# Performance work log

Hardware: AMD Instinct MI355X
Metric: run time of the kernel (lower is better)

The kernel has to match this reference:

```python
import jax, jax.numpy as jnp
import numpy as np

NUM_EMBEDDINGS = 1024
EMBEDDING_DIM = 64
COMMITMENT_COST = 0.25


def setup_inputs() -> dict:
    key = jax.random.key(0)
    k1, k2 = jax.random.split(key)
    inputs = jax.random.normal(k1, (2, 64, 32, 32, 32), dtype=jnp.float32)
    embedding = jax.random.normal(k2, (NUM_EMBEDDINGS, EMBEDDING_DIM), dtype=jnp.float32)
    return {"inputs": inputs, "embedding": embedding}


def reference(inputs, embedding):
    # inputs: [B, C, D, H, W], embedding: [K, C]
    B, C, D, H, W = inputs.shape
    # flatten_permutation = [0, 2, 3, 4, 1] -> [B*D*H*W, C]
    flat_input = jnp.transpose(inputs, (0, 2, 3, 4, 1)).reshape(-1, C)
    # squared euclidean distances [N, K]
    distances = (
        jnp.sum(flat_input**2, axis=1, keepdims=True)
        + jnp.sum(embedding**2, axis=1)[None, :]
        - 2.0 * flat_input @ embedding.T
    )
    # torch.max(-distances, dim=1)[1] == argmin of distances
    encoding_indices = jnp.argmax(-distances, axis=1)  # [N]
    encoding_indices_view = encoding_indices.reshape(B, D, H, W)
    # embed: lookup then quantization_permutation [0, 4, 1, 2, 3] -> channel-first
    quantized = embedding[encoding_indices_view]            # [B, D, H, W, C]
    quantized = jnp.transpose(quantized, (0, 4, 1, 2, 3))   # [B, C, D, H, W]
    # commitment loss: MSE(stop_grad(quantized), inputs)
    loss = COMMITMENT_COST * jnp.mean((jax.lax.stop_gradient(quantized) - inputs) ** 2)
    # straight-through estimator
    quantized_st = inputs + jax.lax.stop_gradient(quantized - inputs)
    # eval path: encodings_sum = zeros(256) (hardcoded in original forward)
    encodings_sum = jnp.zeros(256, dtype=jnp.float32)
    return quantized_st, loss, encoding_indices_view, encodings_sum, embedding
```

## Files before the change

kernel.cpp:

```cpp
#include <hip/hip_runtime.h>
#include <stdint.h>

#define KCODES  1024
#define CDIM    64
#define SPATIAL 32768
#define NPOS    65536
#define NEL     4194304

#define OUT_Q    0
#define OUT_LOSS 4194304
#define OUT_IDX  4194305
#define OUT_SUM  4259841
#define OUT_EMB  4260097

#define NSET16 64
#define SETB   4096
#define EIOFF  262144
#define BPOS   128

typedef _Float16 half8 __attribute__((ext_vector_type(8)));
typedef float    f32x4 __attribute__((ext_vector_type(4)));

__global__ void prep_emb(const float* __restrict__ emb, char* __restrict__ ws,
                         float* __restrict__ out) {
    int gt = blockIdx.x * 256 + threadIdx.x;
    if (gt == 0) out[OUT_LOSS] = 0.f;
    if (gt < 256) out[OUT_SUM + gt] = 0.f;
    {
        float4 v = *(const float4*)(emb + (size_t)gt * 4);
        float* o = out + OUT_EMB + (size_t)gt * 4;
        o[0] = v.x; o[1] = v.y; o[2] = v.z; o[3] = v.w;
    }
    if (gt < 8192) {
        int k = gt >> 3, oct = gt & 7;
        int set = k >> 4, row = k & 15;
        int s = oct >> 2, g = oct & 3;
        const float* e = emb + (size_t)k * CDIM + oct * 8;
        char* rec = ws + (size_t)set * SETB;
        _Float16* hi = (_Float16*)(rec + s * 1024 + ((g << 4) | row) * 16);
        _Float16* lo = (_Float16*)(rec + 2048 + s * 1024 + ((g << 4) | row) * 16);
        float s2 = 0.f;
        half8 hv, lv;
#pragma unroll
        for (int i = 0; i < 8; ++i) {
            float v = e[i];
            s2 = fmaf(v, v, s2);
            _Float16 h = (_Float16)v;
            hv[i] = h;
            lv[i] = (_Float16)(v - (float)h);
        }
        *(half8*)hi = hv;
        *(half8*)lo = lv;
        s2 += __shfl_xor(s2, 1);
        s2 += __shfl_xor(s2, 2);
        s2 += __shfl_xor(s2, 4);
        if (oct == 0) ((float*)(ws + EIOFF))[k] = -0.5f * s2;
    }
}

#define GLDS16(GSRC, LDST)                                                     \
    __builtin_amdgcn_global_load_lds(                                          \
        (const __attribute__((address_space(1))) void*)(GSRC),                 \
        (__attribute__((address_space(3))) void*)(LDST), 16, 0, 0)

__global__ __launch_bounds__(512, 2) void vq_kernel(
        const float* __restrict__ in, const float* __restrict__ emb,
        const char* __restrict__ wsA, float* __restrict__ out) {
    __shared__ __align__(16) char ring[8][2][SETB];
    __shared__ __align__(16) float eiL[KCODES];
    __shared__ float candS[2][BPOS];
    __shared__ int   candK[2][BPOS];
    __shared__ int   kwin[BPOS];
    __shared__ float lred[8];

    const int tid  = threadIdx.x;
    const int lane = tid & 63, wv = tid >> 6;
    const int col  = lane & 15, g = lane >> 4;
    const int pg   = wv & 3, kh = wv >> 2;
    const int p0   = blockIdx.x * BPOS;
    const int b    = p0 >> 15;
    const int s0   = p0 & 32767;
    const float* xin = in + (size_t)b * (CDIM * SPATIAL) + s0;

    float* xl = (float*)&ring[0][0][0];
    {
        int p = tid & 127, cq = tid >> 7;
#pragma unroll
        for (int j = 0; j < 16; ++j) {
            int c = cq * 16 + j;
            xl[c * 129 + p] = xin[(size_t)c * SPATIAL + p];
        }
    }
    eiL[tid]       = ((const float*)(wsA + EIOFF))[tid];
    eiL[tid + 512] = ((const float*)(wsA + EIOFF))[tid + 512];
    __syncthreads();

    half8 bh[2][2], bl[2][2];
#pragma unroll
    for (int nt = 0; nt < 2; ++nt)
#pragma unroll
        for (int s = 0; s < 2; ++s) {
            int pp = pg * 32 + nt * 16 + col;
#pragma unroll
            for (int j = 0; j < 8; ++j) {
                int c = s * 32 + g * 8 + j;
                float v = xl[c * 129 + pp];
                _Float16 hh = (_Float16)v;
                bh[nt][s][j] = hh;
                bl[nt][s][j] = (_Float16)(v - (float)hh);
            }
        }
    __syncthreads();

    const char* myws = wsA + (size_t)kh * 32 * SETB;
    char* slotA = &ring[wv][0][0];
    char* slotB = &ring[wv][1][0];
#define STAGE4(RSET, DST) do {                                                 \
        const char* s_ = myws + (size_t)(RSET) * SETB + lane * 16;             \
        char* d_ = (DST) + lane * 16;                                          \
        GLDS16(s_,        d_);                                                 \
        GLDS16(s_ + 1024, d_ + 1024);                                          \
        GLDS16(s_ + 2048, d_ + 2048);                                          \
        GLDS16(s_ + 3072, d_ + 3072);                                          \
    } while (0)
    STAGE4(0, slotA);

    f32x4 maxS0, maxS1;
    int   maxR0[4], maxR1[4];
#pragma unroll
    for (int r = 0; r < 4; ++r) {
        maxS0[r] = -3.402823466e38f; maxS1[r] = -3.402823466e38f;
        maxR0[r] = 0;                maxR1[r] = 0;
    }

#pragma unroll 1
    for (int r = 0; r < 32; ++r) {
        STAGE4((r + 1) & 31, slotB);
        const int set = kh * 32 + r;
        asm volatile("s_waitcnt vmcnt(4)" ::: "memory");
        f32x4 eiv = *(const f32x4*)&eiL[set * 16 + g * 4];
        const char* ap = slotA + (size_t)lane * 16;
        half8 ah0 = *(const half8*)(ap);
        half8 ah1 = *(const half8*)(ap + 1024);
        half8 al0 = *(const half8*)(ap + 2048);
        half8 al1 = *(const half8*)(ap + 3072);
        f32x4 a0 = __builtin_amdgcn_mfma_f32_16x16x32_f16(ah0, bh[0][0], eiv, 0, 0, 0);
        f32x4 a1 = __builtin_amdgcn_mfma_f32_16x16x32_f16(ah0, bh[1][0], eiv, 0, 0, 0);
        a0 = __builtin_amdgcn_mfma_f32_16x16x32_f16(ah1, bh[0][1], a0, 0, 0, 0);
        a1 = __builtin_amdgcn_mfma_f32_16x16x32_f16(ah1, bh[1][1], a1, 0, 0, 0);
        a0 = __builtin_amdgcn_mfma_f32_16x16x32_f16(ah0, bl[0][0], a0, 0, 0, 0);
        a1 = __builtin_amdgcn_mfma_f32_16x16x32_f16(ah0, bl[1][0], a1, 0, 0, 0);
        a0 = __builtin_amdgcn_mfma_f32_16x16x32_f16(ah1, bl[0][1], a0, 0, 0, 0);
        a1 = __builtin_amdgcn_mfma_f32_16x16x32_f16(ah1, bl[1][1], a1, 0, 0, 0);
        a0 = __builtin_amdgcn_mfma_f32_16x16x32_f16(al0, bh[0][0], a0, 0, 0, 0);
        a1 = __builtin_amdgcn_mfma_f32_16x16x32_f16(al0, bh[1][0], a1, 0, 0, 0);
        a0 = __builtin_amdgcn_mfma_f32_16x16x32_f16(al1, bh[0][1], a0, 0, 0, 0);
        a1 = __builtin_amdgcn_mfma_f32_16x16x32_f16(al1, bh[1][1], a1, 0, 0, 0);
#pragma unroll
        for (int rr = 0; rr < 4; ++rr) {
            if (a0[rr] > maxS0[rr]) { maxS0[rr] = a0[rr]; maxR0[rr] = set; }
            if (a1[rr] > maxS1[rr]) { maxS1[rr] = a1[rr]; maxR1[rr] = set; }
        }
        char* t_ = slotA; slotA = slotB; slotB = t_;
    }
#undef STAGE4

#pragma unroll
    for (int nt = 0; nt < 2; ++nt) {
        float bs = nt ? maxS1[0] : maxS0[0];
        int   bk = (nt ? maxR1[0] : maxR0[0]) * 16 + g * 4;
#pragma unroll
        for (int rr = 1; rr < 4; ++rr) {
            float sc = nt ? maxS1[rr] : maxS0[rr];
            int   kk = (nt ? maxR1[rr] : maxR0[rr]) * 16 + g * 4 + rr;
            if (sc > bs || (sc == bs && kk < bk)) { bs = sc; bk = kk; }
        }
#pragma unroll
        for (int m = 16; m <= 32; m <<= 1) {
            float os = __shfl_xor(bs, m);
            int   ok = __shfl_xor(bk, m);
            if (os > bs || (os == bs && ok < bk)) { bs = os; bk = ok; }
        }
        if (g == 0) {
            candS[kh][pg * 32 + nt * 16 + col] = bs;
            candK[kh][pg * 32 + nt * 16 + col] = bk;
        }
    }
    __syncthreads();

    if (tid < BPOS) {
        float s0v = candS[0][tid], s1v = candS[1][tid];
        int   k0v = candK[0][tid], k1v = candK[1][tid];
        int sel = (s1v > s0v) || (s1v == s0v && k1v < k0v);
        int bkf = sel ? k1v : k0v;
        kwin[tid] = bkf;
        out[OUT_IDX + p0 + tid] = (float)bkf;
    }
    __syncthreads();

    float lsum = 0.f;
    {
        int p = tid & 127, cq = tid >> 7;
        int kk = kwin[p];
        const float* eb = emb + (size_t)kk * CDIM;
        float* q = out + OUT_Q + (size_t)b * (CDIM * SPATIAL) + s0;
#pragma unroll
        for (int j = 0; j < 16; ++j) {
            int c = cq * 16 + j;
            float x = xin[(size_t)c * SPATIAL + p];
            float e = eb[c];
            float d = e - x;
            lsum = fmaf(d, d, lsum);
            q[(size_t)c * SPATIAL + p] = x + d;
        }
    }
#pragma unroll
    for (int off = 32; off > 0; off >>= 1) lsum += __shfl_down(lsum, off);
    if (lane == 0) lred[wv] = lsum;
    __syncthreads();
    if (tid == 0) {
        float t = 0.f;
#pragma unroll
        for (int w = 0; w < 8; ++w) t += lred[w];
        atomicAdd(out + OUT_LOSS, t * (0.25f / (float)NEL));
    }
}

extern "C" void kernel_launch(void* const* d_in, const int* in_sizes, int n_in,
                              void* d_out, int out_size, void* d_ws, size_t ws_size,
                              hipStream_t stream) {
    const float* in  = (const float*)d_in[0];
    const float* emb = (const float*)d_in[1];
    float* out = (float*)d_out;
    char*  ws  = (char*)d_ws;

    prep_emb<<<64, 256, 0, stream>>>(emb, ws, out);
    vq_kernel<<<NPOS / BPOS, 512, 0, stream>>>(in, emb, ws, out);
}
```

Baseline: 44.93 us.

## Halve positions per block, split codebook four ways with shared cooperative staging

Blocks now handle 64 positions instead of 128. The codebook is split across four wave pairs of 16 sets each, and the two waves in a pair cooperatively stage half of each shared 4 KB set into LDS, with block barriers per round. This doubles the grid and shrinks LDS, allowing more resident blocks (launch bounds 8), to improve occupancy and latency hiding. The cost is two s_barriers per round, each set being staged once per pair rather than once per wave, and a 4-way final candidate merge.

New measurement: 104.8 us. +133.2%, slower.

```diff
diff --git a/kernel.cpp b/kernel.cpp
--- a/kernel.cpp
+++ b/kernel.cpp
@@ -13,10 +13,10 @@
 #define OUT_SUM  4259841
 #define OUT_EMB  4260097
 
-#define NSET16 64
 #define SETB   4096
 #define EIOFF  262144
-#define BPOS   128
+#define BPOS   64
+#define NRND   16
 
 typedef _Float16 half8 __attribute__((ext_vector_type(8)));
 typedef float    f32x4 __attribute__((ext_vector_type(4)));
@@ -63,20 +63,20 @@
         (const __attribute__((address_space(1))) void*)(GSRC),                 \
         (__attribute__((address_space(3))) void*)(LDST), 16, 0, 0)
 
-__global__ __launch_bounds__(512, 2) void vq_kernel(
+__global__ __launch_bounds__(512, 8) void vq_kernel(
         const float* __restrict__ in, const float* __restrict__ emb,
         const char* __restrict__ wsA, float* __restrict__ out) {
-    __shared__ __align__(16) char ring[8][2][SETB];
+    __shared__ __align__(16) char ring[4][2][SETB];
     __shared__ __align__(16) float eiL[KCODES];
-    __shared__ float candS[2][BPOS];
-    __shared__ int   candK[2][BPOS];
+    __shared__ float candS[4][BPOS];
+    __shared__ int   candK[4][BPOS];
     __shared__ int   kwin[BPOS];
     __shared__ float lred[8];
 
     const int tid  = threadIdx.x;
     const int lane = tid & 63, wv = tid >> 6;
     const int col  = lane & 15, g = lane >> 4;
-    const int pg   = wv & 3, kh = wv >> 2;
+    const int pg   = wv & 1, kh = wv >> 1;
     const int p0   = blockIdx.x * BPOS;
     const int b    = p0 >> 15;
     const int s0   = p0 & 32767;
@@ -84,11 +84,11 @@
 
     float* xl = (float*)&ring[0][0][0];
     {
-        int p = tid & 127, cq = tid >> 7;
-#pragma unroll
-        for (int j = 0; j < 16; ++j) {
-            int c = cq * 16 + j;
-            xl[c * 129 + p] = xin[(size_t)c * SPATIAL + p];
+        int p = tid & 63, cq = tid >> 6;
+#pragma unroll
+        for (int j = 0; j < 8; ++j) {
+            int c = cq * 8 + j;
+            xl[c * 65 + p] = xin[(size_t)c * SPATIAL + p];
         }
     }
     eiL[tid]       = ((const float*)(wsA + EIOFF))[tid];
@@ -104,7 +104,7 @@
 #pragma unroll
             for (int j = 0; j < 8; ++j) {
                 int c = s * 32 + g * 8 + j;
-                float v = xl[c * 129 + pp];
+                float v = xl[c * 65 + pp];
                 _Float16 hh = (_Float16)v;
                 bh[nt][s][j] = hh;
                 bl[nt][s][j] = (_Float16)(v - (float)hh);
@@ -112,18 +112,14 @@
         }
     __syncthreads();
 
-    const char* myws = wsA + (size_t)kh * 32 * SETB;
-    char* slotA = &ring[wv][0][0];
-    char* slotB = &ring[wv][1][0];
-#define STAGE4(RSET, DST) do {                                                 \
-        const char* s_ = myws + (size_t)(RSET) * SETB + lane * 16;             \
-        char* d_ = (DST) + lane * 16;                                          \
+    const char* myws = wsA + (size_t)kh * NRND * SETB;
+#define STAGE(RSET, SLOT) do {                                                 \
+        const char* s_ = myws + (size_t)(RSET) * SETB + pg * 2048 + lane * 16; \
+        char* d_ = &ring[kh][SLOT][0] + pg * 2048 + lane * 16;                 \
         GLDS16(s_,        d_);                                                 \
         GLDS16(s_ + 1024, d_ + 1024);                                          \
-        GLDS16(s_ + 2048, d_ + 2048);                                          \
-        GLDS16(s_ + 3072, d_ + 3072);                                          \
     } while (0)
-    STAGE4(0, slotA);
+    STAGE(0, 0);
 
     f32x4 maxS0, maxS1;
     int   maxR0[4], maxR1[4];
@@ -134,12 +130,14 @@
     }
 
 #pragma unroll 1
-    for (int r = 0; r < 32; ++r) {
-        STAGE4((r + 1) & 31, slotB);
-        const int set = kh * 32 + r;
-        asm volatile("s_waitcnt vmcnt(4)" ::: "memory");
+    for (int r = 0; r < NRND; ++r) {
+        STAGE((r + 1) & (NRND - 1), (r + 1) & 1);
+        asm volatile("s_waitcnt vmcnt(2)" ::: "memory");
+        __builtin_amdgcn_s_barrier();
+        __builtin_amdgcn_sched_barrier(0);
+        const int set = kh * NRND + r;
         f32x4 eiv = *(const f32x4*)&eiL[set * 16 + g * 4];
-        const char* ap = slotA + (size_t)lane * 16;
+        const char* ap = &ring[kh][r & 1][0] + (size_t)lane * 16;
         half8 ah0 = *(const half8*)(ap);
         half8 ah1 = *(const half8*)(ap + 1024);
         half8 al0 = *(const half8*)(ap + 2048);
@@ -161,9 +159,9 @@
             if (a0[rr] > maxS0[rr]) { maxS0[rr] = a0[rr]; maxR0[rr] = set; }
             if (a1[rr] > maxS1[rr]) { maxS1[rr] = a1[rr]; maxR1[rr] = set; }
         }
-        char* t_ = slotA; slotA = slotB; slotB = t_;
-    }
-#undef STAGE4
+        __builtin_amdgcn_s_barrier();
+    }
+#undef STAGE
 
 #pragma unroll
     for (int nt = 0; nt < 2; ++nt) {
@@ -189,24 +187,28 @@
     __syncthreads();
 
     if (tid < BPOS) {
-        float s0v = candS[0][tid], s1v = candS[1][tid];
-        int   k0v = candK[0][tid], k1v = candK[1][tid];
-        int sel = (s1v > s0v) || (s1v == s0v && k1v < k0v);
-        int bkf = sel ? k1v : k0v;
-        kwin[tid] = bkf;
-        out[OUT_IDX + p0 + tid] = (float)bkf;
+        float bs = candS[0][tid];
+        int   bk = candK[0][tid];
+#pragma unroll
+        for (int w = 1; w < 4; ++w) {
+            float sc = candS[w][tid];
+            int   kk = candK[w][tid];
+            if (sc > bs || (sc == bs && kk < bk)) { bs = sc; bk = kk; }
+        }
+        kwin[tid] = bk;
+        out[OUT_IDX + p0 + tid] = (float)bk;
     }
     __syncthreads();
 
     float lsum = 0.f;
     {
-        int p = tid & 127, cq = tid >> 7;
+        int p = tid & 63, cq = tid >> 6;
         int kk = kwin[p];
         const float* eb = emb + (size_t)kk * CDIM;
         float* q = out + OUT_Q + (size_t)b * (CDIM * SPATIAL) + s0;
 #pragma unroll
-        for (int j = 0; j < 16; ++j) {
-            int c = cq * 16 + j;
+        for (int j = 0; j < 8; ++j) {
+            int c = cq * 8 + j;
             float x = xin[(size_t)c * SPATIAL + p];
             float e = eb[c];
             float d = e - x;
```
